# Kernel tuning notes

Measured on AMD Instinct MI355X. Metric: run time of the kernel, lower is better.

## Reference

```python
import jax, jax.numpy as jnp
import numpy as np
import math

B, Q, H, KVH, D, KV, HID = 2, 1024, 32, 8, 128, 4096, 4096

def rotate_half(x):
    x1, x2 = jnp.split(x, 2, axis=-1)
    return jnp.concatenate([-x2, x1], axis=-1)

def setup_inputs() -> dict:
    key = jax.random.key(0)
    ks = jax.random.split(key, 10)
    inv = 1.0 / math.sqrt(HID)
    return {
        "hidden_states": jax.random.normal(ks[0], (B, Q, HID), dtype=jnp.float32),
        "cos": jax.random.uniform(ks[1], (B, 1, Q, D), dtype=jnp.float32),
        "sin": jax.random.uniform(ks[2], (B, 1, Q, D), dtype=jnp.float32),
        "attention_mask": jnp.zeros((B, 1, Q, KV), dtype=jnp.float32),
        "cache_k": jax.random.normal(ks[3], (B, KVH, KV, D), dtype=jnp.float32),
        "cache_v": jax.random.normal(ks[4], (B, KVH, KV, D), dtype=jnp.float32),
        "sink_ids": jnp.arange(Q, dtype=jnp.int32),
        "Wq": jax.random.normal(ks[5], (H * D, HID), dtype=jnp.float32) * inv,
        "Wk": jax.random.normal(ks[6], (KVH * D, HID), dtype=jnp.float32) * inv,
        "Wv": jax.random.normal(ks[7], (KVH * D, HID), dtype=jnp.float32) * inv,
        "Wo": jax.random.normal(ks[8], (HID, H * D), dtype=jnp.float32) * inv,
    }

def reference(hidden_states, cos, sin, attention_mask, cache_k, cache_v, sink_ids, Wq, Wk, Wv, Wo):
    b, q_len, hid = hidden_states.shape
    d = cos.shape[-1]
    h = Wq.shape[0] // d
    kvh = Wk.shape[0] // d
    n_rep = h // kvh

    # projections -> (b, heads, q, d)
    qs = (hidden_states @ Wq.T).reshape(b, q_len, h, d).transpose(0, 2, 1, 3)
    ks = (hidden_states @ Wk.T).reshape(b, q_len, kvh, d).transpose(0, 2, 1, 3)
    vs = (hidden_states @ Wv.T).reshape(b, q_len, kvh, d).transpose(0, 2, 1, 3)

    # RoPE
    qs = qs * cos + rotate_half(qs) * sin
    ks = ks * cos + rotate_half(ks) * sin

    # sink new K/V into the paged cache at sink_ids, then read back the full cache
    k_cache = cache_k.at[:, :, sink_ids, :].set(ks)
    v_cache = cache_v.at[:, :, sink_ids, :].set(vs)

    # repeat_kv: (b, kvh, kv, d) -> (b, h, kv, d)
    k_full = jnp.repeat(k_cache, n_rep, axis=1)
    v_full = jnp.repeat(v_cache, n_rep, axis=1)

    scores = jnp.einsum('bhqd,bhkd->bhqk', qs, k_full) / math.sqrt(d)
    scores = scores + attention_mask
    attn = jax.nn.softmax(scores.astype(jnp.float32), axis=-1).astype(qs.dtype)
    out = jnp.einsum('bhqk,bhkd->bhqd', attn, v_full)
    out = out.transpose(0, 2, 1, 3).reshape(b, q_len, h * d)
    return out @ Wo.T
```

## Files before the change

### kernel.cpp

```cpp
#include <hip/hip_runtime.h>

typedef __bf16 bf16;
typedef __attribute__((ext_vector_type(8))) __bf16 bf16x8;
typedef __attribute__((ext_vector_type(4))) __bf16 bf16x4;
typedef __attribute__((ext_vector_type(4))) float floatx4;

#define LOG2E 1.4426950408889634f
#define CEXP (0.08838834764831845f * 1.4426950408889634f)

__device__ __forceinline__ void lds16(const void* g, void* l) {
  __builtin_amdgcn_global_load_lds(
      (const __attribute__((address_space(1))) unsigned int*)(unsigned long long)g,
      (__attribute__((address_space(3))) unsigned int*)(unsigned int)(unsigned long long)l,
      16, 0, 0);
}

template <typename CT>
__global__ __launch_bounds__(256) void gemm_bt(const bf16* __restrict__ A,
                                               const bf16* __restrict__ W,
                                               CT* __restrict__ C,
                                               int M, int N, int K) {
  __shared__ bf16 sA[128 * 32];
  __shared__ bf16 sB[128 * 32];
  const int tid = threadIdx.x;
  const int lane = tid & 63;
  const int wave = tid >> 6;
  const int quad = lane >> 4;
  const int l16 = lane & 15;
  const int m0 = blockIdx.y * 128;
  const int n0 = blockIdx.x * 128;
  const int wm = (wave >> 1) * 64;
  const int wn = (wave & 1) * 64;

  floatx4 acc[4][4] = {};

  const int srow = tid >> 2;
  const int cs = tid & 3;
  const int clog = cs ^ ((srow >> 1) & 3);
  const bf16* gA = A + (long)(m0 + srow) * K + clog * 8;
  const bf16* gB = W + (long)(n0 + srow) * K + clog * 8;
  bf16* lA = sA + wave * 512;
  bf16* lB = sB + wave * 512;
  const long step64 = (long)64 * K;
  const int cq = quad ^ ((l16 >> 1) & 3);

  for (int k0 = 0; k0 < K; k0 += 32) {
    lds16(gA, lA);
    lds16(gA + step64, lA + 2048);
    lds16(gB, lB);
    lds16(gB + step64, lB + 2048);
    gA += 32;
    gB += 32;
    __syncthreads();
    bf16x8 af[4], bfr[4];
#pragma unroll
    for (int i = 0; i < 4; ++i)
      af[i] = *(const bf16x8*)(sA + (wm + i * 16 + l16) * 32 + cq * 8);
#pragma unroll
    for (int j = 0; j < 4; ++j)
      bfr[j] = *(const bf16x8*)(sB + (wn + j * 16 + l16) * 32 + cq * 8);
#pragma unroll
    for (int i = 0; i < 4; ++i)
#pragma unroll
      for (int j = 0; j < 4; ++j)
        acc[i][j] = __builtin_amdgcn_mfma_f32_16x16x32_bf16(af[i], bfr[j], acc[i][j], 0, 0, 0);
    __syncthreads();
  }

#pragma unroll
  for (int i = 0; i < 4; ++i) {
    const int row = m0 + wm + i * 16 + quad * 4;
#pragma unroll
    for (int j = 0; j < 4; ++j) {
      const int col = n0 + wn + j * 16 + l16;
#pragma unroll
      for (int r = 0; r < 4; ++r)
        C[(long)(row + r) * N + col] = (CT)acc[i][j][r];
    }
  }
}

__global__ __launch_bounds__(256, 2) void attn(const bf16* __restrict__ qr,
                                               const bf16* __restrict__ kc,
                                               const bf16* __restrict__ vt,
                                               const float* __restrict__ mask,
                                               const int* __restrict__ flag,
                                               bf16* __restrict__ o) {
  __shared__ bf16 sK[2][64 * 128];
  __shared__ bf16 sV[2][128 * 64];
  __shared__ bf16 sP[4 * 32 * 64];
  const int tid = threadIdx.x, lane = tid & 63, wave = tid >> 6;
  const int quad = lane >> 4, l16 = lane & 15;

  int id = blockIdx.x;
  const int kvh = id & 7;
  id >>= 3;
  const int b = id & 1;
  id >>= 1;
  const int h = kvh * 4 + (id & 3);
  const int q0 = (id >> 2) * 128;
  const int qw = q0 + wave * 32;

  const bf16* qbase = qr + ((long)(b * 32 + h) * 1024 + qw) * 128;
  bf16x8 qf[2][4];
#pragma unroll
  for (int qt = 0; qt < 2; ++qt)
#pragma unroll
    for (int ks = 0; ks < 4; ++ks)
      qf[qt][ks] = *(const bf16x8*)(qbase + (long)(qt * 16 + l16) * 128 +
                                    ks * 32 + quad * 8);

  floatx4 oacc[8][2] = {};
  floatx4 lrun4[2] = {};

  const bool use_mask = (*flag != 0);
  const bf16* kbase = kc + (long)(b * 8 + kvh) * 4096 * 128;
  const bf16* vbase = vt + (long)(b * 8 + kvh) * 128 * 4096;
  bf16* sPw = sP + wave * 2048;

  auto stage = [&](int buf, int kt) {
    const int kv0 = kt * 64;
#pragma unroll
    for (int it = 0; it < 4; ++it) {
      const int r0 = wave * 16 + it * 4;
      const int row = r0 + (lane >> 4);
      lds16(kbase + (long)(kv0 + row) * 128 + (((lane & 15) ^ (row & 15)) << 3),
            sK[buf] + r0 * 128);
    }
#pragma unroll
    for (int it = 0; it < 4; ++it) {
      const int r0 = wave * 32 + it * 8;
      const int row = r0 + (lane >> 3);
      lds16(vbase + (long)row * 4096 + kv0 + (((lane & 7) ^ (row & 7)) << 3),
            sV[buf] + r0 * 64);
    }
  };

  stage(0, 0);
  __syncthreads();

  for (int kt = 0; kt < 64; ++kt) {
    const int cur = kt & 1;
    const int kv0 = kt * 64;
    if (kt < 63) stage(cur ^ 1, kt + 1);

    floatx4 s[4][2] = {};
    __builtin_amdgcn_s_setprio(1);
#pragma unroll
    for (int ks = 0; ks < 4; ++ks)
#pragma unroll
      for (int j = 0; j < 4; ++j) {
        const bf16x8 kf = *(const bf16x8*)(sK[cur] + (j * 16 + l16) * 128 +
                                           (((ks * 4 + quad) ^ l16) << 3));
        s[j][0] = __builtin_amdgcn_mfma_f32_16x16x32_bf16(kf, qf[0][ks], s[j][0], 0, 0, 0);
        s[j][1] = __builtin_amdgcn_mfma_f32_16x16x32_bf16(kf, qf[1][ks], s[j][1], 0, 0, 0);
      }
    __builtin_amdgcn_s_setprio(0);

    if (use_mask) {
#pragma unroll
      for (int qt = 0; qt < 2; ++qt)
#pragma unroll
        for (int j = 0; j < 4; ++j)
#pragma unroll
          for (int r = 0; r < 4; ++r) {
            const int q = qw + qt * 16 + l16;
            const int kv = kv0 + j * 16 + quad * 4 + r;
            s[j][qt][r] += mask[((long)b * 1024 + q) * 4096 + kv] * LOG2E;
          }
    }

#pragma unroll
    for (int qt = 0; qt < 2; ++qt)
#pragma unroll
      for (int j = 0; j < 4; ++j) {
        bf16x4 pk;
        floatx4 pv;
#pragma unroll
        for (int r = 0; r < 4; ++r) {
          pv[r] = exp2f(s[j][qt][r]);
          pk[r] = (bf16)pv[r];
        }
        lrun4[qt] += pv;
        *(bf16x4*)(sPw + (qt * 16 + l16) * 64 +
                   (((j * 2 + (quad >> 1)) ^ (l16 & 7)) << 3) + ((quad & 1) << 2)) = pk;
      }

    __builtin_amdgcn_s_setprio(1);
#pragma unroll
    for (int kc2 = 0; kc2 < 2; ++kc2) {
      const int ph = ((kc2 * 4 + quad) ^ (l16 & 7)) << 3;
      const bf16x8 pf0 = *(const bf16x8*)(sPw + l16 * 64 + ph);
      const bf16x8 pf1 = *(const bf16x8*)(sPw + (16 + l16) * 64 + ph);
#pragma unroll
      for (int mt = 0; mt < 8; ++mt) {
        const bf16x8 vf = *(const bf16x8*)(sV[cur] + (mt * 16 + l16) * 64 + ph);
        oacc[mt][0] = __builtin_amdgcn_mfma_f32_16x16x32_bf16(vf, pf0, oacc[mt][0], 0, 0, 0);
        oacc[mt][1] = __builtin_amdgcn_mfma_f32_16x16x32_bf16(vf, pf1, oacc[mt][1], 0, 0, 0);
      }
    }
    __builtin_amdgcn_s_setprio(0);

    __syncthreads();
  }

#pragma unroll
  for (int qt = 0; qt < 2; ++qt) {
    float ls = (lrun4[qt][0] + lrun4[qt][1]) + (lrun4[qt][2] + lrun4[qt][3]);
    ls += __shfl_xor(ls, 16, 64);
    ls += __shfl_xor(ls, 32, 64);
    const float inv = 1.f / ls;
    const int q = qw + qt * 16 + l16;
    bf16* op = o + ((long)(b * 1024 + q) * 32 + h) * 128 + quad * 4;
#pragma unroll
    for (int mt = 0; mt < 8; ++mt) {
      bf16x4 ov;
#pragma unroll
      for (int r = 0; r < 4; ++r) ov[r] = (bf16)(oacc[mt][qt][r] * inv);
      *(bf16x4*)(op + mt * 16) = ov;
    }
  }
}

__global__ void zeroflag(int* f) { *f = 0; }

__global__ void f2b4(const floatx4* __restrict__ in, bf16x4* __restrict__ out) {
  const long i = (long)blockIdx.x * 256 + threadIdx.x;
  const floatx4 v = in[i];
  bf16x4 o;
  o[0] = (bf16)v[0]; o[1] = (bf16)v[1]; o[2] = (bf16)v[2]; o[3] = (bf16)v[3];
  out[i] = o;
}

__global__ void maskchk(const floatx4* __restrict__ m, int* __restrict__ flag) {
  const long i = (long)blockIdx.x * 256 + threadIdx.x;
  const floatx4 v = m[i];
  if (v[0] != 0.f || v[1] != 0.f || v[2] != 0.f || v[3] != 0.f) atomicOr(flag, 1);
}

__global__ void vtrans(const float* __restrict__ v, bf16* __restrict__ vt) {
  __shared__ float t[32][33];
  const int bk = blockIdx.z;
  const int kv0 = blockIdx.x * 32, d0 = blockIdx.y * 32;
  const int tx = threadIdx.x, ty = threadIdx.y;
  const float* src = v + ((long)bk * 4096 + kv0) * 128 + d0;
#pragma unroll
  for (int k = 0; k < 4; ++k) t[ty * 4 + k][tx] = src[(ty * 4 + k) * 128 + tx];
  __syncthreads();
  bf16* dst = vt + ((long)bk * 128 + d0) * 4096 + kv0;
#pragma unroll
  for (int k = 0; k < 4; ++k) dst[(ty * 4 + k) * 4096 + tx] = (bf16)t[tx][ty * 4 + k];
}

__global__ void rope_q(const bf16* __restrict__ qkv, const float* __restrict__ cosp,
                       const float* __restrict__ sinp, bf16* __restrict__ qrope) {
  const long idx = (long)blockIdx.x * 256 + threadIdx.x;
  const int d = (int)idx & 127;
  const int q = (int)(idx >> 7) & 1023;
  const int h = (int)(idx >> 17) & 31;
  const int b = (int)(idx >> 22);
  const long qrow = ((long)b * 1024 + q) * 6144 + h * 128;
  const float x = (float)qkv[qrow + d];
  const float y = (float)qkv[qrow + (d ^ 64)];
  const long ci = ((long)b * 1024 + q) * 128 + d;
  const float rh = (d < 64) ? -y : y;
  qrope[idx] = (bf16)((x * cosp[ci] + rh * sinp[ci]) * CEXP);
}

__global__ void rope_k(const bf16* __restrict__ qkv, const float* __restrict__ cosp,
                       const float* __restrict__ sinp, const int* __restrict__ sink,
                       bf16* __restrict__ kcb) {
  const long idx = (long)blockIdx.x * 256 + threadIdx.x;
  const int d = (int)idx & 127;
  const int kvh = (int)(idx >> 7) & 7;
  const int q = (int)(idx >> 10) & 1023;
  const int b = (int)(idx >> 20);
  const long krow = ((long)b * 1024 + q) * 6144 + 4096 + kvh * 128;
  const float x = (float)qkv[krow + d];
  const float y = (float)qkv[krow + (d ^ 64)];
  const long ci = ((long)b * 1024 + q) * 128 + d;
  const float rh = (d < 64) ? -y : y;
  const int sk = sink[q];
  kcb[(((long)b * 8 + kvh) * 4096 + sk) * 128 + d] = (bf16)(x * cosp[ci] + rh * sinp[ci]);
}

__global__ void scat_v(const bf16* __restrict__ qkv, const int* __restrict__ sink,
                       bf16* __restrict__ vtb) {
  const long idx = (long)blockIdx.x * 256 + threadIdx.x;
  const int q = (int)idx & 1023;
  const int d = (int)(idx >> 10) & 127;
  const int kvh = (int)(idx >> 17) & 7;
  const int b = (int)(idx >> 20);
  const int sk = sink[q];
  const bf16 val = qkv[((long)b * 1024 + q) * 6144 + 5120 + kvh * 128 + d];
  vtb[(((long)b * 8 + kvh) * 128 + d) * 4096 + sk] = val;
}

extern "C" void kernel_launch(void* const* d_in, const int* in_sizes, int n_in,
                              void* d_out, int out_size, void* d_ws, size_t ws_size,
                              hipStream_t stream) {
  const float* hid  = (const float*)d_in[0];
  const float* cosp = (const float*)d_in[1];
  const float* sinp = (const float*)d_in[2];
  const float* mask = (const float*)d_in[3];
  const float* ck   = (const float*)d_in[4];
  const float* cv   = (const float*)d_in[5];
  const int*   sink = (const int*)d_in[6];
  const float* Wq   = (const float*)d_in[7];
  const float* Wk   = (const float*)d_in[8];
  const float* Wv   = (const float*)d_in[9];
  const float* Wo   = (const float*)d_in[10];
  float* out = (float*)d_out;

  char* ws = (char*)d_ws;
  bf16* wqkv  = (bf16*)(ws);
  bf16* hidb  = (bf16*)(ws + 50331648);
  bf16* qkvb  = (bf16*)(ws + 67108864);
  bf16* qrope = (bf16*)(ws + 92274688);
  bf16* kcb   = (bf16*)(ws + 109051904);
  bf16* vtb   = (bf16*)(ws + 125829120);
  bf16* ob    = (bf16*)(ws + 142606336);
  int*  flag  = (int*)(ws + 159383552);
  bf16* wob   = (bf16*)(ws + 50331648);

  zeroflag<<<1, 1, 0, stream>>>(flag);

  f2b4<<<8192, 256, 0, stream>>>((const floatx4*)hid, (bf16x4*)hidb);
  f2b4<<<16384, 256, 0, stream>>>((const floatx4*)Wq, (bf16x4*)wqkv);
  f2b4<<<4096, 256, 0, stream>>>((const floatx4*)Wk, (bf16x4*)(wqkv + 16777216));
  f2b4<<<4096, 256, 0, stream>>>((const floatx4*)Wv, (bf16x4*)(wqkv + 20971520));
  f2b4<<<8192, 256, 0, stream>>>((const floatx4*)ck, (bf16x4*)kcb);
  maskchk<<<8192, 256, 0, stream>>>((const floatx4*)mask, flag);
  vtrans<<<dim3(128, 4, 16), dim3(32, 8), 0, stream>>>(cv, vtb);

  gemm_bt<bf16><<<dim3(48, 16), 256, 0, stream>>>(hidb, wqkv, qkvb, 2048, 6144, 4096);

  rope_q<<<32768, 256, 0, stream>>>(qkvb, cosp, sinp, qrope);
  rope_k<<<8192, 256, 0, stream>>>(qkvb, cosp, sinp, sink, kcb);
  scat_v<<<8192, 256, 0, stream>>>(qkvb, sink, vtb);

  f2b4<<<16384, 256, 0, stream>>>((const floatx4*)Wo, (bf16x4*)wob);

  attn<<<512, 256, 0, stream>>>(qrope, kcb, vtb, mask, flag, ob);

  gemm_bt<float><<<dim3(32, 16), 256, 0, stream>>>(ob, wob, out, 2048, 4096, 4096);

  (void)in_sizes; (void)n_in; (void)out_size; (void)ws_size;
}
```

Baseline: 705.1 us.

## Fuse conversion and RoPE/scatter kernels and vectorize V transpose

Merges the five fp32-to-bf16 conversion launches and the mask check into one block-indexed prep kernel. It also combines rope_q, rope_k and the V scatter into a single vectorized kernel that handles 4 or 8 elements per thread. The V transpose now uses 64-row tiles and writes bf16x8 vectors. The goal is fewer launches and better memory access width, at the cost of branchy block dispatch and more complex indexing.

After: 683.1 us. 3.1% less time.

```diff
diff --git a/kernel.cpp b/kernel.cpp
--- a/kernel.cpp
+++ b/kernel.cpp
@@ -224,6 +224,33 @@
 
 __global__ void zeroflag(int* f) { *f = 0; }
 
+__global__ void prep(const floatx4* __restrict__ hid, const floatx4* __restrict__ wq,
+                     const floatx4* __restrict__ wk, const floatx4* __restrict__ wv,
+                     const floatx4* __restrict__ ck, const floatx4* __restrict__ mask,
+                     bf16x4* __restrict__ hidb, bf16x4* __restrict__ wqkvb,
+                     bf16x4* __restrict__ kcb, int* __restrict__ flag) {
+  const int bid = blockIdx.x;
+  const int tid = threadIdx.x;
+  if (bid >= 40960) {
+    const long i = (long)(bid - 40960) * 256 + tid;
+    const floatx4 v = mask[i];
+    if (v[0] != 0.f || v[1] != 0.f || v[2] != 0.f || v[3] != 0.f) atomicOr(flag, 1);
+    return;
+  }
+  const floatx4* in;
+  bf16x4* out;
+  long i;
+  if (bid < 8192)       { i = (long)bid * 256 + tid;           in = hid; out = hidb; }
+  else if (bid < 24576) { i = (long)(bid - 8192) * 256 + tid;  in = wq;  out = wqkvb; }
+  else if (bid < 28672) { i = (long)(bid - 24576) * 256 + tid; in = wk;  out = wqkvb + 4194304; }
+  else if (bid < 32768) { i = (long)(bid - 28672) * 256 + tid; in = wv;  out = wqkvb + 5242880; }
+  else                  { i = (long)(bid - 32768) * 256 + tid; in = ck;  out = kcb; }
+  const floatx4 v = in[i];
+  bf16x4 o;
+  o[0] = (bf16)v[0]; o[1] = (bf16)v[1]; o[2] = (bf16)v[2]; o[3] = (bf16)v[3];
+  out[i] = o;
+}
+
 __global__ void f2b4(const floatx4* __restrict__ in, bf16x4* __restrict__ out) {
   const long i = (long)blockIdx.x * 256 + threadIdx.x;
   const floatx4 v = in[i];
@@ -232,68 +259,92 @@
   out[i] = o;
 }
 
-__global__ void maskchk(const floatx4* __restrict__ m, int* __restrict__ flag) {
-  const long i = (long)blockIdx.x * 256 + threadIdx.x;
-  const floatx4 v = m[i];
-  if (v[0] != 0.f || v[1] != 0.f || v[2] != 0.f || v[3] != 0.f) atomicOr(flag, 1);
-}
-
 __global__ void vtrans(const float* __restrict__ v, bf16* __restrict__ vt) {
-  __shared__ float t[32][33];
+  __shared__ float t[64][33];
   const int bk = blockIdx.z;
-  const int kv0 = blockIdx.x * 32, d0 = blockIdx.y * 32;
-  const int tx = threadIdx.x, ty = threadIdx.y;
+  const int kv0 = blockIdx.x * 64, d0 = blockIdx.y * 32;
+  const int tid = threadIdx.x;
   const float* src = v + ((long)bk * 4096 + kv0) * 128 + d0;
-#pragma unroll
-  for (int k = 0; k < 4; ++k) t[ty * 4 + k][tx] = src[(ty * 4 + k) * 128 + tx];
+  const int rr = tid >> 5, cc = tid & 31;
+#pragma unroll
+  for (int p = 0; p < 8; ++p)
+    t[p * 8 + rr][cc] = src[(long)(p * 8 + rr) * 128 + cc];
   __syncthreads();
-  bf16* dst = vt + ((long)bk * 128 + d0) * 4096 + kv0;
-#pragma unroll
-  for (int k = 0; k < 4; ++k) dst[(ty * 4 + k) * 4096 + tx] = (bf16)t[tx][ty * 4 + k];
-}
-
-__global__ void rope_q(const bf16* __restrict__ qkv, const float* __restrict__ cosp,
-                       const float* __restrict__ sinp, bf16* __restrict__ qrope) {
-  const long idx = (long)blockIdx.x * 256 + threadIdx.x;
-  const int d = (int)idx & 127;
-  const int q = (int)(idx >> 7) & 1023;
-  const int h = (int)(idx >> 17) & 31;
-  const int b = (int)(idx >> 22);
-  const long qrow = ((long)b * 1024 + q) * 6144 + h * 128;
-  const float x = (float)qkv[qrow + d];
-  const float y = (float)qkv[qrow + (d ^ 64)];
-  const long ci = ((long)b * 1024 + q) * 128 + d;
-  const float rh = (d < 64) ? -y : y;
-  qrope[idx] = (bf16)((x * cosp[ci] + rh * sinp[ci]) * CEXP);
-}
-
-__global__ void rope_k(const bf16* __restrict__ qkv, const float* __restrict__ cosp,
-                       const float* __restrict__ sinp, const int* __restrict__ sink,
-                       bf16* __restrict__ kcb) {
-  const long idx = (long)blockIdx.x * 256 + threadIdx.x;
-  const int d = (int)idx & 127;
-  const int kvh = (int)(idx >> 7) & 7;
-  const int q = (int)(idx >> 10) & 1023;
-  const int b = (int)(idx >> 20);
-  const long krow = ((long)b * 1024 + q) * 6144 + 4096 + kvh * 128;
-  const float x = (float)qkv[krow + d];
-  const float y = (float)qkv[krow + (d ^ 64)];
-  const long ci = ((long)b * 1024 + q) * 128 + d;
-  const float rh = (d < 64) ? -y : y;
-  const int sk = sink[q];
-  kcb[(((long)b * 8 + kvh) * 4096 + sk) * 128 + d] = (bf16)(x * cosp[ci] + rh * sinp[ci]);
-}
-
-__global__ void scat_v(const bf16* __restrict__ qkv, const int* __restrict__ sink,
-                       bf16* __restrict__ vtb) {
-  const long idx = (long)blockIdx.x * 256 + threadIdx.x;
-  const int q = (int)idx & 1023;
-  const int d = (int)(idx >> 10) & 127;
-  const int kvh = (int)(idx >> 17) & 7;
-  const int b = (int)(idx >> 20);
-  const int sk = sink[q];
-  const bf16 val = qkv[((long)b * 1024 + q) * 6144 + 5120 + kvh * 128 + d];
-  vtb[(((long)b * 8 + kvh) * 128 + d) * 4096 + sk] = val;
+  const int rowD = tid >> 3, oct = tid & 7;
+  bf16x8 o;
+#pragma unroll
+  for (int i = 0; i < 8; ++i) o[i] = (bf16)t[oct * 8 + i][rowD];
+  *(bf16x8*)(vt + ((long)bk * 128 + d0 + rowD) * 4096 + kv0 + oct * 8) = o;
+}
+
+__global__ void ropes(const bf16* __restrict__ qkv, const float* __restrict__ cosp,
+                      const float* __restrict__ sinp, const int* __restrict__ sink,
+                      bf16* __restrict__ qrope, bf16* __restrict__ kcb,
+                      bf16* __restrict__ vtb) {
+  const int bid = blockIdx.x;
+  const int tid = threadIdx.x;
+  if (bid < 4096) {
+    const int t = bid * 256 + tid;
+    const int j = t & 15;
+    const int q = (t >> 4) & 1023;
+    const int h = (t >> 14) & 31;
+    const int b = t >> 19;
+    const long qrow = ((long)b * 1024 + q) * 6144 + h * 128;
+    const bf16x4 x = *(const bf16x4*)(qkv + qrow + j * 4);
+    const bf16x4 y = *(const bf16x4*)(qkv + qrow + 64 + j * 4);
+    const long ci = ((long)b * 1024 + q) * 128 + j * 4;
+    const floatx4 cl = *(const floatx4*)(cosp + ci);
+    const floatx4 sl = *(const floatx4*)(sinp + ci);
+    const floatx4 ch = *(const floatx4*)(cosp + ci + 64);
+    const floatx4 sh = *(const floatx4*)(sinp + ci + 64);
+    bf16x4 xo, yo;
+#pragma unroll
+    for (int i = 0; i < 4; ++i) {
+      const float xf = (float)x[i], yf = (float)y[i];
+      xo[i] = (bf16)((xf * cl[i] - yf * sl[i]) * CEXP);
+      yo[i] = (bf16)((yf * ch[i] + xf * sh[i]) * CEXP);
+    }
+    bf16* ob = qrope + ((long)(b * 32 + h) * 1024 + q) * 128 + j * 4;
+    *(bf16x4*)ob = xo;
+    *(bf16x4*)(ob + 64) = yo;
+  } else if (bid < 5120) {
+    const int t = (bid - 4096) * 256 + tid;
+    const int j = t & 15;
+    const int q = (t >> 4) & 1023;
+    const int kvh = (t >> 14) & 7;
+    const int b = t >> 17;
+    const long krow = ((long)b * 1024 + q) * 6144 + 4096 + kvh * 128;
+    const bf16x4 x = *(const bf16x4*)(qkv + krow + j * 4);
+    const bf16x4 y = *(const bf16x4*)(qkv + krow + 64 + j * 4);
+    const long ci = ((long)b * 1024 + q) * 128 + j * 4;
+    const floatx4 cl = *(const floatx4*)(cosp + ci);
+    const floatx4 sl = *(const floatx4*)(sinp + ci);
+    const floatx4 ch = *(const floatx4*)(cosp + ci + 64);
+    const floatx4 sh = *(const floatx4*)(sinp + ci + 64);
+    bf16x4 xo, yo;
+#pragma unroll
+    for (int i = 0; i < 4; ++i) {
+      const float xf = (float)x[i], yf = (float)y[i];
+      xo[i] = (bf16)(xf * cl[i] - yf * sl[i]);
+      yo[i] = (bf16)(yf * ch[i] + xf * sh[i]);
+    }
+    const int sk = sink[q];
+    bf16* ob = kcb + (((long)b * 8 + kvh) * 4096 + sk) * 128 + j * 4;
+    *(bf16x4*)ob = xo;
+    *(bf16x4*)(ob + 64) = yo;
+  } else {
+    const int t = (bid - 5120) * 256 + tid;
+    const int j = t & 15;
+    const int q = (t >> 4) & 1023;
+    const int kvh = (t >> 14) & 7;
+    const int b = t >> 17;
+    const bf16x8 v = *(const bf16x8*)(qkv + ((long)b * 1024 + q) * 6144 + 5120 +
+                                      kvh * 128 + j * 8);
+    const int sk = sink[q];
+    bf16* dst = vtb + (((long)b * 8 + kvh) * 128 + j * 8) * 4096 + sk;
+#pragma unroll
+    for (int i = 0; i < 8; ++i) dst[(long)i * 4096] = v[i];
+  }
 }
 
 extern "C" void kernel_launch(void* const* d_in, const int* in_sizes, int n_in,
@@ -325,19 +376,16 @@
 
   zeroflag<<<1, 1, 0, stream>>>(flag);
 
-  f2b4<<<8192, 256, 0, stream>>>((const floatx4*)hid, (bf16x4*)hidb);
-  f2b4<<<16384, 256, 0, stream>>>((const floatx4*)Wq, (bf16x4*)wqkv);
-  f2b4<<<4096, 256, 0, stream>>>((const floatx4*)Wk, (bf16x4*)(wqkv + 16777216));
-  f2b4<<<4096, 256, 0, stream>>>((const floatx4*)Wv, (bf16x4*)(wqkv + 20971520));
-  f2b4<<<8192, 256, 0, stream>>>((const floatx4*)ck, (bf16x4*)kcb);
-  maskchk<<<8192, 256, 0, stream>>>((const floatx4*)mask, flag);
-  vtrans<<<dim3(128, 4, 16), dim3(32, 8), 0, stream>>>(cv, vtb);
+  prep<<<49152, 256, 0, stream>>>((const floatx4*)hid, (const floatx4*)Wq,
+                                  (const floatx4*)Wk, (const floatx4*)Wv,
+                                  (const floatx4*)ck, (const floatx4*)mask,
+                                  (bf16x4*)hidb, (bf16x4*)wqkv, (bf16x4*)kcb, flag);
+
+  vtrans<<<dim3(64, 4, 16), 256, 0, stream>>>(cv, vtb);
 
   gemm_bt<bf16><<<dim3(48, 16), 256, 0, stream>>>(hidb, wqkv, qkvb, 2048, 6144, 4096);
 
-  rope_q<<<32768, 256, 0, stream>>>(qkvb, cosp, sinp, qrope);
-  rope_k<<<8192, 256, 0, stream>>>(qkvb, cosp, sinp, sink, kcb);
-  scat_v<<<8192, 256, 0, stream>>>(qkvb, sink, vtb);
+  ropes<<<6144, 256, 0, stream>>>(qkvb, cosp, sinp, sink, qrope, kcb, vtb);
 
   f2b4<<<16384, 256, 0, stream>>>((const floatx4*)Wo, (bf16x4*)wob);
 
```
